# Optimization experiments

Measured on AMD Instinct MI355X. Metric: run time of the kernel, lower is better.

The kernel has to match this reference:

```python
import jax, jax.numpy as jnp
import numpy as np

K = 16  # memory_topk

def signed_abs_softmax(x, axis=-1):
    # sign(x) * softmax(|x|): the module's 'signed_abs_softmax' route/edge compression
    return jnp.sign(x) * jax.nn.softmax(jnp.abs(x), axis=axis)

def unit_norm(v, eps=1e-6):
    return v / (jnp.linalg.norm(v, axis=-1, keepdims=True) + eps)

def setup_inputs() -> dict:
    key = jax.random.key(0)
    ks = jax.random.split(key, 7)
    B, T, D, S, R = 8, 2048, 512, 2048, 64
    std = 0.02
    return {
        "x": jax.random.normal(ks[0], (B, T, D), jnp.float32),
        "init_state": std * jax.random.normal(ks[1], (S,), jnp.float32),
        "init_val": std * jax.random.normal(ks[2], (S, D), jnp.float32),
        "route_a": std * jax.random.normal(ks[3], (D, R), jnp.float32),
        "route_b": std * jax.random.normal(ks[4], (R, S), jnp.float32),
        "pair_a": std * jax.random.normal(ks[5], (D, R), jnp.float32),
        "pair_b": std * jax.random.normal(ks[6], (D, R), jnp.float32),
    }

def reference(x, init_state, init_val, route_a, route_b, pair_a, pair_b):
    B, T, D = x.shape
    S = init_val.shape[0]
    b_idx = jnp.arange(B)[:, None, None]

    # --- initialize memory level (signed-softmax state, unit-norm values) ---
    state = jnp.broadcast_to(signed_abs_softmax(init_state), (B, S))
    val = jnp.broadcast_to(unit_norm(init_val), (B, S, D))

    # --- SparseTransition write: topk route tokens -> slots, scatter-add ---
    scores = jnp.einsum('btd,dr,rs->bts', x, route_a, route_b)   # [B,T,S] low-rank route
    _, idx = jax.lax.top_k(jnp.abs(scores), K)                    # [B,T,K] topk by magnitude
    g = jnp.take_along_axis(scores, idx, axis=-1)                 # signed gathered scores
    w = signed_abs_softmax(g, axis=-1)                            # route compression
    v = unit_norm(x)                                              # use_direction_only=True
    val_delta = jnp.zeros((B, S, D), x.dtype).at[b_idx, idx].add(w[..., None] * v[:, :, None, :])
    state_delta = jnp.zeros((B, S), x.dtype).at[b_idx, idx].add(jax.nn.softplus(g))
    state = signed_abs_softmax(state + state_delta, axis=-1)      # merge='add' + signed softmax state
    val = unit_norm(val + val_delta)                              # merge='add' + unit-norm values

    # --- SparsePropagation: topk pairwise edges among slots, residual mix ---
    q = jnp.einsum('bsd,dr->bsr', val, pair_a)
    kk = jnp.einsum('bsd,dr->bsr', val, pair_b)
    p = jnp.einsum('bir,bjr->bij', q, kk)                         # [B,S,S] low-rank pairwise
    _, eidx = jax.lax.top_k(jnp.abs(p), K)                        # [B,S,K] topk edges per slot
    pe = jnp.take_along_axis(p, eidx, axis=-1)
    ew = signed_abs_softmax(pe, axis=-1)                          # edge compression
    nbr = val[b_idx, eidx]                                        # [B,S,K,D] gather neighbor values
    delta = jnp.einsum('bsk,bskd->bsd', ew, nbr)
    val = unit_norm(val + delta)                                  # residual + unit-norm

    # pack (state, val) into one array: [B,S,1+D]
    return jnp.concatenate([state[..., None], val], axis=-1)
```

## Files before the change

### kernel.cpp

```cpp
#include <hip/hip_runtime.h>
#include <cmath>

namespace {
constexpr int B = 8;
constexpr int T = 2048;
constexpr int D = 512;
constexpr int S = 2048;
constexpr int R = 64;
constexpr int KTOP = 16;
constexpr int NT = 4;
constexpr int NR = 16;
constexpr int NI = 8;
constexpr int CAP = 256;

__device__ __forceinline__ float signf(float v) {
    return (v > 0.f) ? 1.f : ((v < 0.f) ? -1.f : 0.f);
}

__device__ __forceinline__ void topk16_row(float* __restrict__ row,
                                           unsigned long long* __restrict__ cand,
                                           int lane, float& myg, int& myj) {
    const float4* p4 = (const float4*)row;
    float lmax = 0.f;
#pragma unroll
    for (int i = 0; i < 8; i++) {
        float4 v = p4[lane + 64 * i];
        lmax = fmaxf(lmax, fmaxf(fmaxf(fabsf(v.x), fabsf(v.y)),
                                 fmaxf(fabsf(v.z), fabsf(v.w))));
    }
    {
        float v = lmax;
#pragma unroll
        for (int size = 2; size <= 64; size <<= 1) {
#pragma unroll
            for (int stride = size >> 1; stride > 0; stride >>= 1) {
                float o = __shfl_xor(v, stride, 64);
                bool takeMax = ((lane & size) == 0) == ((lane & stride) == 0);
                v = takeMax ? fmaxf(v, o) : fminf(v, o);
            }
        }
        lmax = __shfl(v, 15);
    }
    float t = lmax;
    int cnt = 0;
#pragma unroll
    for (int i = 0; i < 8; i++) {
        float4 v = p4[lane + 64 * i];
        cnt += (fabsf(v.x) >= t) + (fabsf(v.y) >= t) +
               (fabsf(v.z) >= t) + (fabsf(v.w) >= t);
    }
    int off = cnt;
#pragma unroll
    for (int d = 1; d < 64; d <<= 1) {
        int o = __shfl_up(off, d, 64);
        if (lane >= d) off += o;
    }
    int total = __shfl(off, 63);
    int base = off - cnt;

    if (total <= 64) {
        int pos = base;
#pragma unroll
        for (int i = 0; i < 8; i++) {
            float4 v = p4[lane + 64 * i];
            int jb = 4 * (lane + 64 * i);
            float c[4] = {v.x, v.y, v.z, v.w};
#pragma unroll
            for (int cc = 0; cc < 4; cc++) {
                if (fabsf(c[cc]) >= t) {
                    unsigned ab = __float_as_uint(c[cc]) & 0x7fffffffu;
                    cand[pos++] = ((unsigned long long)ab << 11) |
                                  (unsigned)(2047 - (jb + cc));
                }
            }
        }
        unsigned long long key = (lane < total) ? cand[lane] : 0ull;
#pragma unroll
        for (int size = 2; size <= 64; size <<= 1) {
#pragma unroll
            for (int stride = size >> 1; stride > 0; stride >>= 1) {
                unsigned long long o = __shfl_xor((long long)key, stride, 64);
                bool takeMax = ((lane & size) == 0) == ((lane & stride) == 0);
                key = (takeMax == (key > o)) ? key : o;
            }
        }
        myg = 0.f; myj = 0;
        if (lane < KTOP) {
            myj = 2047 - (int)(key & 2047ull);
            myg = row[myj];
        }
    } else {
        myg = 0.f; myj = 0;
        for (int k = 0; k < KTOP; k++) {
            float bv = -1.f, bs = 0.f; int bj = 0;
#pragma unroll
            for (int i = 0; i < 8; i++) {
                float4 v = p4[lane + 64 * i];
                int jb = 4 * (lane + 64 * i);
                { float a = fabsf(v.x); if (a > bv) { bv = a; bs = v.x; bj = jb; } }
                { float a = fabsf(v.y); if (a > bv) { bv = a; bs = v.y; bj = jb + 1; } }
                { float a = fabsf(v.z); if (a > bv) { bv = a; bs = v.z; bj = jb + 2; } }
                { float a = fabsf(v.w); if (a > bv) { bv = a; bs = v.w; bj = jb + 3; } }
            }
#pragma unroll
            for (int off2 = 32; off2 > 0; off2 >>= 1) {
                float ov = __shfl_xor(bv, off2, 64);
                float os = __shfl_xor(bs, off2, 64);
                int   oj = __shfl_xor(bj, off2, 64);
                if (ov > bv || (ov == bv && oj < bj)) { bv = ov; bs = os; bj = oj; }
            }
            if (lane == k) { myg = bs; myj = bj; }
            if (lane == 0) row[bj] = 0.f;
        }
    }
}
}

__global__ void k_init_state(const float* __restrict__ init_state,
                             float* __restrict__ state_ws) {
    int b = blockIdx.x;
    int tid = threadIdx.x;
    __shared__ float red[256];
    float m = -1e30f;
    for (int s = tid; s < S; s += 256) m = fmaxf(m, fabsf(init_state[s]));
    red[tid] = m; __syncthreads();
    for (int off = 128; off > 0; off >>= 1) {
        if (tid < off) red[tid] = fmaxf(red[tid], red[tid + off]);
        __syncthreads();
    }
    m = red[0]; __syncthreads();
    float sum = 0.f;
    for (int s = tid; s < S; s += 256) sum += expf(fabsf(init_state[s]) - m);
    red[tid] = sum; __syncthreads();
    for (int off = 128; off > 0; off >>= 1) {
        if (tid < off) red[tid] += red[tid + off];
        __syncthreads();
    }
    float inv = 1.0f / red[0];
    for (int s = tid; s < S; s += 256) {
        float v = init_state[s];
        state_ws[(size_t)b * S + s] = signf(v) * expf(fabsf(v) - m) * inv;
    }
}

__global__ void k_bcast(const float* __restrict__ init_val,
                        float* __restrict__ val1) {
    int wv = threadIdx.x >> 6;
    int lane = threadIdx.x & 63;
    int blk = ((blockIdx.x & 7) << 9) | (blockIdx.x >> 3);
    int row = blk * 4 + wv;
    int s = row & (S - 1);
    const float4* src = (const float4*)(init_val + (size_t)s * D);
    float4 v0 = src[lane], v1 = src[lane + 64];
    float ss = v0.x * v0.x + v0.y * v0.y + v0.z * v0.z + v0.w * v0.w
             + v1.x * v1.x + v1.y * v1.y + v1.z * v1.z + v1.w * v1.w;
#pragma unroll
    for (int off = 32; off > 0; off >>= 1) ss += __shfl_xor(ss, off, 64);
    float sc = 1.0f / (sqrtf(ss) + 1e-6f);
    v0.x *= sc; v0.y *= sc; v0.z *= sc; v0.w *= sc;
    v1.x *= sc; v1.y *= sc; v1.z *= sc; v1.w *= sc;
    float4* dst = (float4*)(val1 + (size_t)row * D);
    dst[lane] = v0; dst[lane + 64] = v1;
}

__global__ void __launch_bounds__(256) k_score(const float* __restrict__ x,
                                               const float* __restrict__ route_a,
                                               const float* __restrict__ route_b,
                                               float* __restrict__ val1,
                                               float* __restrict__ state_ws,
                                               float* __restrict__ coef,
                                               int* __restrict__ bincount,
                                               int* __restrict__ binlist) {
    __shared__ __align__(16) char smem[NT * S * 4];
    __shared__ __align__(16) float xr[NT][R];
    __shared__ __align__(16) char umem[4096];
    float (*sc)[S] = (float(*)[S])smem;
    float (*xs)[D] = (float(*)[D])smem;
    float (*red4)[256] = (float(*)[256])umem;
    unsigned long long (*cand)[64] = (unsigned long long(*)[64])umem;

    int tid = threadIdx.x;
    int lane = tid & 63, wv = tid >> 6;
    int blk = ((blockIdx.x & 7) << 9) | (blockIdx.x >> 3);
    int tb = blk * NT;
    int b = tb >> 11;
    int t0 = tb & (T - 1);

    {
        const float4* xg = (const float4*)(x + (size_t)tb * D);
        float4* xls = (float4*)&xs[0][0];
        xls[tid] = xg[tid];
        xls[tid + 256] = xg[tid + 256];
    }
    __syncthreads();

    {
        int r = lane, grp = wv;
        float acc[NT] = {0.f, 0.f, 0.f, 0.f};
        for (int d0 = grp * 128; d0 < grp * 128 + 128; d0 += 4) {
            float a0 = route_a[(size_t)(d0 + 0) * R + r];
            float a1 = route_a[(size_t)(d0 + 1) * R + r];
            float a2 = route_a[(size_t)(d0 + 2) * R + r];
            float a3 = route_a[(size_t)(d0 + 3) * R + r];
#pragma unroll
            for (int tt = 0; tt < NT; tt++) {
                float4 xv = *(const float4*)&xs[tt][d0];
                acc[tt] += xv.x * a0 + xv.y * a1 + xv.z * a2 + xv.w * a3;
            }
        }
#pragma unroll
        for (int tt = 0; tt < NT; tt++) red4[tt][tid] = acc[tt];
        __syncthreads();
        {
            int tt2 = tid >> 6, r2 = tid & 63;
            xr[tt2][r2] = red4[tt2][r2] + red4[tt2][64 + r2] +
                          red4[tt2][128 + r2] + red4[tt2][192 + r2];
        }
        __syncthreads();
    }

    {
        const float4* rb4 = (const float4*)route_b;
#pragma unroll
        for (int i = 0; i < 2; i++) {
            int j4 = tid + 256 * i;
            float4 acc[NT];
#pragma unroll
            for (int tt = 0; tt < NT; tt++) acc[tt] = make_float4(0.f, 0.f, 0.f, 0.f);
            for (int r0 = 0; r0 < R; r0 += 4) {
                float4 xv[NT];
#pragma unroll
                for (int tt = 0; tt < NT; tt++) xv[tt] = *(const float4*)&xr[tt][r0];
#define SCORE_STEP(dr, comp)                                                   \
                {                                                              \
                    float4 bv = rb4[(size_t)(r0 + dr) * (S / 4) + j4];         \
                    _Pragma("unroll")                                          \
                    for (int tt = 0; tt < NT; tt++) {                          \
                        float c = xv[tt].comp;                                 \
                        acc[tt].x += c * bv.x; acc[tt].y += c * bv.y;          \
                        acc[tt].z += c * bv.z; acc[tt].w += c * bv.w;          \
                    }                                                          \
                }
                SCORE_STEP(0, x) SCORE_STEP(1, y) SCORE_STEP(2, z) SCORE_STEP(3, w)
#undef SCORE_STEP
            }
#pragma unroll
            for (int tt = 0; tt < NT; tt++)
                ((float4*)&sc[tt][0])[j4] = acc[tt];
        }
    }
    __syncthreads();

    int tt = wv;
    int tloc = t0 + tt;
    int tglob = tb + tt;

    float xinv;
    {
        const float4* xg = (const float4*)(x + (size_t)tglob * D);
        float4 x0 = xg[lane], x1 = xg[lane + 64];
        float ss = x0.x * x0.x + x0.y * x0.y + x0.z * x0.z + x0.w * x0.w
                 + x1.x * x1.x + x1.y * x1.y + x1.z * x1.z + x1.w * x1.w;
#pragma unroll
        for (int off = 32; off > 0; off >>= 1) ss += __shfl_xor(ss, off, 64);
        xinv = 1.0f / (sqrtf(ss) + 1e-6f);
    }

    float myg; int myj;
    topk16_row(&sc[tt][0], &cand[wv][0], lane, myg, myj);

    float m = __shfl(fabsf(myg), 0);
    float e = (lane < KTOP) ? expf(fabsf(myg) - m) : 0.f;
    float esum = e;
#pragma unroll
    for (int off = 8; off > 0; off >>= 1) esum += __shfl_xor(esum, off, 64);
    esum = __shfl(esum, 0);
    float w = signf(myg) * e / esum;
    float coefv = w * xinv;

    unsigned long long ovf = 0ull;
    int pos = 0;
    if (lane < KTOP) {
        float sp = (myg > 20.f) ? myg : log1pf(expf(myg));
        atomicAdd(&state_ws[(size_t)b * S + myj], sp);
        pos = atomicAdd(&bincount[(size_t)b * S + myj], 1);
        if (pos < CAP) {
            binlist[((size_t)b * S + myj) * CAP + pos] = (tloc << 4) | lane;
            coef[(size_t)tglob * KTOP + lane] = coefv;
        }
    }
    ovf = __ballot(lane < KTOP && pos >= CAP);
    while (ovf) {
        int src = __ffsll(ovf) - 1;
        int j = __shfl(myj, src);
        float c = __shfl(coefv, src);
        float* dst = val1 + ((size_t)b * S + j) * D;
        const float* xrow = x + (size_t)tglob * D;
#pragma unroll
        for (int i = 0; i < 8; i++)
            atomicAdd(&dst[lane + 64 * i], c * xrow[lane + 64 * i]);
        ovf &= ovf - 1;
    }
}

__global__ void __launch_bounds__(256) k_accum(const float* __restrict__ x,
                                               const float* __restrict__ coef,
                                               const int* __restrict__ bincount,
                                               const int* __restrict__ binlist,
                                               float* __restrict__ val1) {
    int lane = threadIdx.x & 63, wv = threadIdx.x >> 6;
    int blk = ((blockIdx.x & 7) << 9) | (blockIdx.x >> 3);
    int row = blk * 4 + wv;
    int b = row >> 11;
    float4* vp4 = (float4*)(val1 + (size_t)row * D);
    float4 a0 = vp4[lane], a1 = vp4[lane + 64];
    int n = bincount[row]; if (n > CAP) n = CAP;
    const int* lp = binlist + (size_t)row * CAP;
    for (int base = 0; base < n; base += 64) {
        int mm = n - base; if (mm > 64) mm = 64;
        int ent = 0; float cc = 0.f;
        if (lane < mm) {
            ent = lp[base + lane];
            cc = coef[((size_t)b * T + (ent >> 4)) * KTOP + (ent & 15)];
        }
        for (int k = 0; k < mm; k++) {
            int e2 = __shfl(ent, k);
            float c = __shfl(cc, k);
            const float4* xp4 = (const float4*)(x + ((size_t)b * T + (e2 >> 4)) * D);
            float4 v0 = xp4[lane], v1 = xp4[lane + 64];
            a0.x += c * v0.x; a0.y += c * v0.y; a0.z += c * v0.z; a0.w += c * v0.w;
            a1.x += c * v1.x; a1.y += c * v1.y; a1.z += c * v1.z; a1.w += c * v1.w;
        }
    }
    float ss = a0.x * a0.x + a0.y * a0.y + a0.z * a0.z + a0.w * a0.w
             + a1.x * a1.x + a1.y * a1.y + a1.z * a1.z + a1.w * a1.w;
#pragma unroll
    for (int off = 32; off > 0; off >>= 1) ss += __shfl_xor(ss, off, 64);
    float sc = 1.0f / (sqrtf(ss) + 1e-6f);
    a0.x *= sc; a0.y *= sc; a0.z *= sc; a0.w *= sc;
    a1.x *= sc; a1.y *= sc; a1.z *= sc; a1.w *= sc;
    vp4[lane] = a0; vp4[lane + 64] = a1;
}

__global__ void k_state_final(const float* __restrict__ state_ws,
                              float* __restrict__ out) {
    int b = blockIdx.x;
    int tid = threadIdx.x;
    __shared__ float red[256];
    const float* sp = state_ws + (size_t)b * S;
    float m = -1e30f;
    for (int s = tid; s < S; s += 256) m = fmaxf(m, fabsf(sp[s]));
    red[tid] = m; __syncthreads();
    for (int off = 128; off > 0; off >>= 1) {
        if (tid < off) red[tid] = fmaxf(red[tid], red[tid + off]);
        __syncthreads();
    }
    m = red[0]; __syncthreads();
    float sum = 0.f;
    for (int s = tid; s < S; s += 256) sum += expf(fabsf(sp[s]) - m);
    red[tid] = sum; __syncthreads();
    for (int off = 128; off > 0; off >>= 1) {
        if (tid < off) red[tid] += red[tid + off];
        __syncthreads();
    }
    float inv = 1.0f / red[0];
    for (int s = tid; s < S; s += 256) {
        float v = sp[s];
        out[((size_t)b * S + s) * (D + 1)] = signf(v) * expf(fabsf(v) - m) * inv;
    }
}

__global__ void __launch_bounds__(256) k_qk(const float* __restrict__ val1,
                                            const float* __restrict__ pair_a,
                                            const float* __restrict__ pair_b,
                                            float* __restrict__ q,
                                            float* __restrict__ kkT) {
    __shared__ __align__(16) float vrow[NR][D];
    __shared__ float redq[256];
    __shared__ float redk[256];
    int tid = threadIdx.x;
    int blk = ((blockIdx.x & 7) << 7) | (blockIdx.x >> 3);
    int rowbase = blk * NR;
    int b = rowbase >> 11;
    int sbase = rowbase & (S - 1);
    {
        const float4* gv = (const float4*)(val1 + (size_t)rowbase * D);
        float4* lv = (float4*)&vrow[0][0];
        for (int i = tid; i < NR * D / 4; i += 256) lv[i] = gv[i];
    }
    __syncthreads();
    int r = tid & 63, grp = tid >> 6;
    float accq[NR], acck[NR];
#pragma unroll
    for (int rr = 0; rr < NR; rr++) { accq[rr] = 0.f; acck[rr] = 0.f; }
    for (int d0 = grp * 128; d0 < grp * 128 + 128; d0 += 4) {
#pragma unroll
        for (int dd = 0; dd < 4; dd++) {
            float a  = pair_a[(size_t)(d0 + dd) * R + r];
            float bb = pair_b[(size_t)(d0 + dd) * R + r];
#pragma unroll
            for (int rr = 0; rr < NR; rr++) {
                float v = vrow[rr][d0 + dd];
                accq[rr] += v * a;
                acck[rr] += v * bb;
            }
        }
    }
    for (int rr = 0; rr < NR; rr++) {
        redq[tid] = accq[rr]; redk[tid] = acck[rr];
        __syncthreads();
        if (tid < 64) {
            float qv = redq[tid] + redq[tid + 64] + redq[tid + 128] + redq[tid + 192];
            float kv = redk[tid] + redk[tid + 64] + redk[tid + 128] + redk[tid + 192];
            q[(size_t)(rowbase + rr) * R + tid] = qv;
            kkT[((size_t)b * R + tid) * S + (sbase + rr)] = kv;
        }
        __syncthreads();
    }
}

__global__ void __launch_bounds__(512) k_pscore(const float* __restrict__ q,
                                                const float* __restrict__ kkT,
                                                int* __restrict__ eidx,
                                                float* __restrict__ ew_g) {
    __shared__ __align__(16) float prow[NI][S];
    __shared__ __align__(16) float qrow[NI][R];
    __shared__ unsigned long long cand[NI][64];

    int tid = threadIdx.x;
    int lane = tid & 63, wv = tid >> 6;
    int blk = ((blockIdx.x & 7) << 8) | (blockIdx.x >> 3);
    int ibase = blk * NI;
    int b = ibase >> 11;

    {
        int rr = tid >> 6, r = tid & 63;
        qrow[rr][r] = q[(size_t)(ibase + rr) * R + r];
    }
    __syncthreads();

    {
        const float4* kk4 = (const float4*)(kkT + (size_t)b * R * S);
        int j4 = tid;
        float4 acc[NI];
#pragma unroll
        for (int rr = 0; rr < NI; rr++) acc[rr] = make_float4(0.f, 0.f, 0.f, 0.f);
        for (int r0 = 0; r0 < R; r0 += 4) {
            float4 qv[NI];
#pragma unroll
            for (int rr = 0; rr < NI; rr++) qv[rr] = *(const float4*)&qrow[rr][r0];
#define P_STEP(dr, comp)                                                       \
            {                                                                  \
                float4 kv = kk4[(size_t)(r0 + dr) * (S / 4) + j4];             \
                _Pragma("unroll")                                              \
                for (int rr = 0; rr < NI; rr++) {                              \
                    float c = qv[rr].comp;                                     \
                    acc[rr].x += c * kv.x; acc[rr].y += c * kv.y;              \
                    acc[rr].z += c * kv.z; acc[rr].w += c * kv.w;              \
                }                                                              \
            }
            P_STEP(0, x) P_STEP(1, y) P_STEP(2, z) P_STEP(3, w)
#undef P_STEP
        }
#pragma unroll
        for (int rr = 0; rr < NI; rr++)
            ((float4*)&prow[rr][0])[j4] = acc[rr];
    }
    __syncthreads();

    int row = ibase + wv;
    float myg; int myj;
    topk16_row(&prow[wv][0], &cand[wv][0], lane, myg, myj);

    float m = __shfl(fabsf(myg), 0);
    float e = (lane < KTOP) ? expf(fabsf(myg) - m) : 0.f;
    float esum = e;
#pragma unroll
    for (int off = 8; off > 0; off >>= 1) esum += __shfl_xor(esum, off, 64);
    esum = __shfl(esum, 0);
    float myw = signf(myg) * e / esum;

    if (lane < KTOP) {
        eidx[(size_t)row * KTOP + lane] = myj;
        ew_g[(size_t)row * KTOP + lane] = myw;
    }
}

__global__ void __launch_bounds__(256) k_mix(const int* __restrict__ eidx,
                                             const float* __restrict__ ew_g,
                                             const float* __restrict__ val1,
                                             float* __restrict__ out) {
    int lane = threadIdx.x & 63, wv = threadIdx.x >> 6;
    int blk = ((blockIdx.x & 7) << 9) | (blockIdx.x >> 3);
    int row = blk * 4 + wv;
    int b = row >> 11;

    int e_i = 0; float e_w = 0.f;
    if (lane < KTOP) {
        e_i = eidx[(size_t)row * KTOP + lane];
        e_w = ew_g[(size_t)row * KTOP + lane];
    }

    const float4* self4 = (const float4*)(val1 + (size_t)row * D);
    float4 a0 = self4[lane], a1 = self4[lane + 64];
#pragma unroll
    for (int k = 0; k < KTOP; k++) {
        int j = __shfl(e_i, k);
        float w = __shfl(e_w, k);
        const float4* nb4 = (const float4*)(val1 + ((size_t)b * S + j) * D);
        float4 v0 = nb4[lane], v1 = nb4[lane + 64];
        a0.x += w * v0.x; a0.y += w * v0.y; a0.z += w * v0.z; a0.w += w * v0.w;
        a1.x += w * v1.x; a1.y += w * v1.y; a1.z += w * v1.z; a1.w += w * v1.w;
    }
    float ss = a0.x * a0.x + a0.y * a0.y + a0.z * a0.z + a0.w * a0.w
             + a1.x * a1.x + a1.y * a1.y + a1.z * a1.z + a1.w * a1.w;
#pragma unroll
    for (int off = 32; off > 0; off >>= 1) ss += __shfl_xor(ss, off, 64);
    float sc = 1.0f / (sqrtf(ss) + 1e-6f);
    float* op = out + (size_t)row * (D + 1) + 1;
    int d0 = 4 * lane;
    op[d0 + 0] = a0.x * sc; op[d0 + 1] = a0.y * sc;
    op[d0 + 2] = a0.z * sc; op[d0 + 3] = a0.w * sc;
    op[256 + d0 + 0] = a1.x * sc; op[256 + d0 + 1] = a1.y * sc;
    op[256 + d0 + 2] = a1.z * sc; op[256 + d0 + 3] = a1.w * sc;
}

extern "C" void kernel_launch(void* const* d_in, const int* in_sizes, int n_in,
                              void* d_out, int out_size, void* d_ws, size_t ws_size,
                              hipStream_t stream) {
    (void)in_sizes; (void)n_in; (void)out_size; (void)ws_size;
    const float* x          = (const float*)d_in[0];
    const float* init_state = (const float*)d_in[1];
    const float* init_val   = (const float*)d_in[2];
    const float* route_a    = (const float*)d_in[3];
    const float* route_b    = (const float*)d_in[4];
    const float* pair_a     = (const float*)d_in[5];
    const float* pair_b     = (const float*)d_in[6];
    float* out = (float*)d_out;

    float* ws       = (float*)d_ws;
    float* val1     = ws;
    float* q        = val1 + (size_t)B * S * D;
    float* kkT      = q    + (size_t)B * S * R;
    float* state_ws = kkT  + (size_t)B * R * S;
    float* coef     = state_ws + (size_t)B * S;
    int*   bincount = (int*)(coef + (size_t)B * T * KTOP);
    int*   binlist  = bincount + (size_t)B * S;
    int*   eidx     = binlist;
    float* ew       = (float*)(binlist + (size_t)B * S * KTOP);

    hipMemsetAsync(bincount, 0, (size_t)B * S * sizeof(int), stream);
    hipLaunchKernelGGL(k_init_state, dim3(B), dim3(256), 0, stream, init_state, state_ws);
    hipLaunchKernelGGL(k_bcast, dim3(B * S / 4), dim3(256), 0, stream, init_val, val1);
    hipLaunchKernelGGL(k_score, dim3(B * T / NT), dim3(256), 0, stream,
                       x, route_a, route_b, val1, state_ws, coef, bincount, binlist);
    hipLaunchKernelGGL(k_state_final, dim3(B), dim3(256), 0, stream, state_ws, out);
    hipLaunchKernelGGL(k_accum, dim3(B * S / 4), dim3(256), 0, stream,
                       x, coef, bincount, binlist, val1);
    hipLaunchKernelGGL(k_qk, dim3(B * S / NR), dim3(256), 0, stream,
                       val1, pair_a, pair_b, q, kkT);
    hipLaunchKernelGGL(k_pscore, dim3(B * S / NI), dim3(512), 0, stream,
                       q, kkT, eidx, ew);
    hipLaunchKernelGGL(k_mix, dim3(B * S / 4), dim3(256), 0, stream,
                       eidx, ew, val1, out);
}
```

Measured before the change: 433.2 us.

## Score eight tokens per 512-thread block and prefetch next row in accumulate

Doubles the tokens handled per score block from four to eight with 512 threads, so each route_b and route_a load is reused across more tokens and the block count halves. Scratch shared memory is reused for the reduction buffer, which needs an extra barrier. The accumulate kernel also software-prefetches the next gathered x row before doing the FMAs on the current one, to hide gather latency. Costs are higher shared memory and register pressure per block, which may lower occupancy.

New measurement: 413.1 us. -4.6%, faster.

```diff
diff --git a/kernel.cpp b/kernel.cpp
--- a/kernel.cpp
+++ b/kernel.cpp
@@ -8,7 +8,7 @@
 constexpr int S = 2048;
 constexpr int R = 64;
 constexpr int KTOP = 16;
-constexpr int NT = 4;
+constexpr int NT = 8;
 constexpr int NR = 16;
 constexpr int NI = 8;
 constexpr int CAP = 256;
@@ -163,41 +163,42 @@
     dst[lane] = v0; dst[lane + 64] = v1;
 }
 
-__global__ void __launch_bounds__(256) k_score(const float* __restrict__ x,
-                                               const float* __restrict__ route_a,
-                                               const float* __restrict__ route_b,
-                                               float* __restrict__ val1,
-                                               float* __restrict__ state_ws,
-                                               float* __restrict__ coef,
-                                               int* __restrict__ bincount,
-                                               int* __restrict__ binlist) {
+__global__ void __launch_bounds__(512, 4) k_score(const float* __restrict__ x,
+                                                  const float* __restrict__ route_a,
+                                                  const float* __restrict__ route_b,
+                                                  float* __restrict__ val1,
+                                                  float* __restrict__ state_ws,
+                                                  float* __restrict__ coef,
+                                                  int* __restrict__ bincount,
+                                                  int* __restrict__ binlist) {
     __shared__ __align__(16) char smem[NT * S * 4];
     __shared__ __align__(16) float xr[NT][R];
-    __shared__ __align__(16) char umem[4096];
+    __shared__ unsigned long long cand[NT][64];
     float (*sc)[S] = (float(*)[S])smem;
     float (*xs)[D] = (float(*)[D])smem;
-    float (*red4)[256] = (float(*)[256])umem;
-    unsigned long long (*cand)[64] = (unsigned long long(*)[64])umem;
+    float (*red4)[512] = (float(*)[512])smem;
 
     int tid = threadIdx.x;
     int lane = tid & 63, wv = tid >> 6;
-    int blk = ((blockIdx.x & 7) << 9) | (blockIdx.x >> 3);
+    int blk = ((blockIdx.x & 7) << 8) | (blockIdx.x >> 3);
     int tb = blk * NT;
     int b = tb >> 11;
     int t0 = tb & (T - 1);
 
     {
         const float4* xg = (const float4*)(x + (size_t)tb * D);
-        float4* xls = (float4*)&xs[0][0];
+        float4* xls = (float4*)smem;
         xls[tid] = xg[tid];
-        xls[tid + 256] = xg[tid + 256];
+        xls[tid + 512] = xg[tid + 512];
     }
     __syncthreads();
 
     {
-        int r = lane, grp = wv;
-        float acc[NT] = {0.f, 0.f, 0.f, 0.f};
-        for (int d0 = grp * 128; d0 < grp * 128 + 128; d0 += 4) {
+        int r = lane;
+        float acc[NT];
+#pragma unroll
+        for (int tt = 0; tt < NT; tt++) acc[tt] = 0.f;
+        for (int d0 = wv * 64; d0 < wv * 64 + 64; d0 += 4) {
             float a0 = route_a[(size_t)(d0 + 0) * R + r];
             float a1 = route_a[(size_t)(d0 + 1) * R + r];
             float a2 = route_a[(size_t)(d0 + 2) * R + r];
@@ -208,46 +209,46 @@
                 acc[tt] += xv.x * a0 + xv.y * a1 + xv.z * a2 + xv.w * a3;
             }
         }
+        __syncthreads();
 #pragma unroll
         for (int tt = 0; tt < NT; tt++) red4[tt][tid] = acc[tt];
         __syncthreads();
         {
             int tt2 = tid >> 6, r2 = tid & 63;
-            xr[tt2][r2] = red4[tt2][r2] + red4[tt2][64 + r2] +
-                          red4[tt2][128 + r2] + red4[tt2][192 + r2];
+            float s = 0.f;
+#pragma unroll
+            for (int g = 0; g < 8; g++) s += red4[tt2][g * 64 + r2];
+            xr[tt2][r2] = s;
         }
         __syncthreads();
     }
 
     {
         const float4* rb4 = (const float4*)route_b;
-#pragma unroll
-        for (int i = 0; i < 2; i++) {
-            int j4 = tid + 256 * i;
-            float4 acc[NT];
-#pragma unroll
-            for (int tt = 0; tt < NT; tt++) acc[tt] = make_float4(0.f, 0.f, 0.f, 0.f);
-            for (int r0 = 0; r0 < R; r0 += 4) {
-                float4 xv[NT];
-#pragma unroll
-                for (int tt = 0; tt < NT; tt++) xv[tt] = *(const float4*)&xr[tt][r0];
+        int j4 = tid;
+        float4 acc[NT];
+#pragma unroll
+        for (int tt = 0; tt < NT; tt++) acc[tt] = make_float4(0.f, 0.f, 0.f, 0.f);
+        for (int r0 = 0; r0 < R; r0 += 4) {
+            float4 xv[NT];
+#pragma unroll
+            for (int tt = 0; tt < NT; tt++) xv[tt] = *(const float4*)&xr[tt][r0];
 #define SCORE_STEP(dr, comp)                                                   \
-                {                                                              \
-                    float4 bv = rb4[(size_t)(r0 + dr) * (S / 4) + j4];         \
-                    _Pragma("unroll")                                          \
-                    for (int tt = 0; tt < NT; tt++) {                          \
-                        float c = xv[tt].comp;                                 \
-                        acc[tt].x += c * bv.x; acc[tt].y += c * bv.y;          \
-                        acc[tt].z += c * bv.z; acc[tt].w += c * bv.w;          \
-                    }                                                          \
-                }
-                SCORE_STEP(0, x) SCORE_STEP(1, y) SCORE_STEP(2, z) SCORE_STEP(3, w)
+            {                                                                  \
+                float4 bv = rb4[(size_t)(r0 + dr) * (S / 4) + j4];             \
+                _Pragma("unroll")                                              \
+                for (int tt = 0; tt < NT; tt++) {                              \
+                    float c = xv[tt].comp;                                     \
+                    acc[tt].x += c * bv.x; acc[tt].y += c * bv.y;              \
+                    acc[tt].z += c * bv.z; acc[tt].w += c * bv.w;              \
+                }                                                              \
+            }
+            SCORE_STEP(0, x) SCORE_STEP(1, y) SCORE_STEP(2, z) SCORE_STEP(3, w)
 #undef SCORE_STEP
-            }
-#pragma unroll
-            for (int tt = 0; tt < NT; tt++)
-                ((float4*)&sc[tt][0])[j4] = acc[tt];
-        }
+        }
+#pragma unroll
+        for (int tt = 0; tt < NT; tt++)
+            ((float4*)&sc[tt][0])[j4] = acc[tt];
     }
     __syncthreads();
 
@@ -323,13 +324,19 @@
             ent = lp[base + lane];
             cc = coef[((size_t)b * T + (ent >> 4)) * KTOP + (ent & 15)];
         }
+        int e0 = __shfl(ent, 0);
+        const float4* xp4 = (const float4*)(x + ((size_t)b * T + (e0 >> 4)) * D);
+        float4 v0 = xp4[lane], v1 = xp4[lane + 64];
         for (int k = 0; k < mm; k++) {
-            int e2 = __shfl(ent, k);
             float c = __shfl(cc, k);
-            const float4* xp4 = (const float4*)(x + ((size_t)b * T + (e2 >> 4)) * D);
-            float4 v0 = xp4[lane], v1 = xp4[lane + 64];
-            a0.x += c * v0.x; a0.y += c * v0.y; a0.z += c * v0.z; a0.w += c * v0.w;
-            a1.x += c * v1.x; a1.y += c * v1.y; a1.z += c * v1.z; a1.w += c * v1.w;
+            float4 c0 = v0, c1 = v1;
+            if (k + 1 < mm) {
+                int e2 = __shfl(ent, k + 1);
+                const float4* np4 = (const float4*)(x + ((size_t)b * T + (e2 >> 4)) * D);
+                v0 = np4[lane]; v1 = np4[lane + 64];
+            }
+            a0.x += c * c0.x; a0.y += c * c0.y; a0.z += c * c0.z; a0.w += c * c0.w;
+            a1.x += c * c1.x; a1.y += c * c1.y; a1.z += c * c1.z; a1.w += c * c1.w;
         }
     }
     float ss = a0.x * a0.x + a0.y * a0.y + a0.z * a0.z + a0.w * a0.w
@@ -552,7 +559,7 @@
     hipMemsetAsync(bincount, 0, (size_t)B * S * sizeof(int), stream);
     hipLaunchKernelGGL(k_init_state, dim3(B), dim3(256), 0, stream, init_state, state_ws);
     hipLaunchKernelGGL(k_bcast, dim3(B * S / 4), dim3(256), 0, stream, init_val, val1);
-    hipLaunchKernelGGL(k_score, dim3(B * T / NT), dim3(256), 0, stream,
+    hipLaunchKernelGGL(k_score, dim3(B * T / NT), dim3(512), 0, stream,
                        x, route_a, route_b, val1, state_ws, coef, bincount, binlist);
     hipLaunchKernelGGL(k_state_final, dim3(B), dim3(256), 0, stream, state_ws, out);
     hipLaunchKernelGGL(k_accum, dim3(B * S / 4), dim3(256), 0, stream,
```
